# Kernel optimization log

Measured on AMD Instinct MI355X. Metric: run time of the kernel, lower is better.

The kernel has to match this reference:

```python
import jax, jax.numpy as jnp
import numpy as np

B, T, N, E = 4, 16, 1024, 16384
F_IN, H, FF, NH, L, C = 128, 256, 1024, 8, 2, 10
HD = H // NH
EPS = 1e-5


def setup_inputs() -> dict:
    key = jax.random.key(0)
    ks = jax.random.split(key, 12)
    g = lambda k, s: jax.random.normal(k, s, dtype=jnp.float32) * 0.02
    return {
        "x": jax.random.normal(ks[0], (B, T, N, F_IN), dtype=jnp.float32),
        "edge_index": jax.random.randint(ks[1], (B, T, 2, E), 0, N, dtype=jnp.int32),
        # GraphSAGE layer 1 (PyG SAGEConv: lin_l on mean-aggregated neighbors, lin_r on self)
        "sage1_Wl": g(ks[2], (F_IN, H)), "sage1_bl": jnp.zeros((H,), jnp.float32),
        "sage1_Wr": g(ks[3], (F_IN, H)),
        # GraphSAGE layer 2
        "sage2_Wl": g(ks[4], (H, H)), "sage2_bl": jnp.zeros((H,), jnp.float32),
        "sage2_Wr": g(ks[5], (H, H)),
        # TransformerEncoder, stacked over L layers
        "Wqkv": g(ks[6], (L, H, 3 * H)), "bqkv": jnp.zeros((L, 3 * H), jnp.float32),
        "Wo": g(ks[7], (L, H, H)), "bo": jnp.zeros((L, H), jnp.float32),
        "ln1_s": jnp.ones((L, H), jnp.float32), "ln1_b": jnp.zeros((L, H), jnp.float32),
        "W1": g(ks[8], (L, H, FF)), "b1": jnp.zeros((L, FF), jnp.float32),
        "W2": g(ks[9], (L, FF, H)), "b2": jnp.zeros((L, H), jnp.float32),
        "ln2_s": jnp.ones((L, H), jnp.float32), "ln2_b": jnp.zeros((L, H), jnp.float32),
        # final classifier
        "fc_W": g(ks[10], (H, C)), "fc_b": jnp.zeros((C,), jnp.float32),
    }


def _sage_conv(x, src, dst, Wl, bl, Wr):
    # mean neighbor aggregation: for each target node, mean of source features
    deg = jax.ops.segment_sum(jnp.ones((E,), x.dtype), dst, num_segments=N)
    agg = jax.ops.segment_sum(x[src], dst, num_segments=N)  # [N, F]
    agg = agg / jnp.clip(deg, 1.0)[:, None]
    return agg @ Wl + bl + x @ Wr


def _layernorm(x, s, b):
    m = jnp.mean(x, axis=-1, keepdims=True)
    v = jnp.var(x, axis=-1, keepdims=True)
    return (x - m) * jax.lax.rsqrt(v + EPS) * s + b


def _encoder_layer(h, Wqkv, bqkv, Wo, bo, ln1_s, ln1_b, W1, b1, W2, b2, ln2_s, ln2_b):
    # h: [B, T, H] -- post-norm (PyTorch default norm_first=False), relu FFN
    qkv = h @ Wqkv + bqkv  # [B, T, 3H]
    q, k, v = jnp.split(qkv, 3, axis=-1)
    sp = lambda t: t.reshape(B, T, NH, HD).transpose(0, 2, 1, 3)  # [B, NH, T, HD]
    q, k, v = sp(q), sp(k), sp(v)
    scores = jnp.einsum("bhqd,bhkd->bhqk", q, k) / np.sqrt(HD).astype(np.float32)
    attn = jax.nn.softmax(scores, axis=-1)
    ctx = jnp.einsum("bhqk,bhkd->bhqd", attn, v)
    ctx = ctx.transpose(0, 2, 1, 3).reshape(B, T, H)
    h = _layernorm(h + ctx @ Wo + bo, ln1_s, ln1_b)
    ffn = jax.nn.relu(h @ W1 + b1) @ W2 + b2
    return _layernorm(h + ffn, ln2_s, ln2_b)


def reference(x, edge_index, sage1_Wl, sage1_bl, sage1_Wr, sage2_Wl, sage2_bl,
              sage2_Wr, Wqkv, bqkv, Wo, bo, ln1_s, ln1_b, W1, b1, W2, b2,
              ln2_s, ln2_b, fc_W, fc_b):
    xf = x.reshape(B * T, N, F_IN)
    ef = edge_index.reshape(B * T, 2, E)

    def per_graph(xg, eg):
        src, dst = eg[0], eg[1]
        h = jax.nn.relu(_sage_conv(xg, src, dst, sage1_Wl, sage1_bl, sage1_Wr))
        h = _sage_conv(h, src, dst, sage2_Wl, sage2_bl, sage2_Wr)
        return jnp.mean(h, axis=0)  # mean-pool over nodes -> [H]

    emb = jax.vmap(per_graph)(xf, ef).reshape(B, T, H)

    h = emb
    for l in range(L):
        h = _encoder_layer(h, Wqkv[l], bqkv[l], Wo[l], bo[l], ln1_s[l], ln1_b[l],
                           W1[l], b1[l], W2[l], b2[l], ln2_s[l], ln2_b[l])
    return h[:, -1, :] @ fc_W + fc_b  # [B, C]
```

## Files before the change

### kernel.cpp

```cpp
#include <hip/hip_runtime.h>
#include <hip/hip_bf16.h>

#define Bc 4
#define Tc 16
#define Nc 1024
#define Ec 16384
#define FIN 128
#define Hc 256
#define FFc 1024
#define NHc 8
#define Lc 2
#define HDc 32
#define Gc 64
#define EPSc 1e-5f

typedef __bf16 v8bf __attribute__((ext_vector_type(8)));
typedef float v4f __attribute__((ext_vector_type(4)));

__global__ void pack_w_kernel(const float* __restrict__ Wl, const float* __restrict__ Wr,
                              __bf16* __restrict__ pH, __bf16* __restrict__ pL) {
    int bid = blockIdx.x;
    int t = threadIdx.x;
    int lane = t >> 3, j = t & 7;
    int kc = bid >> 4, nt = bid & 15;
    int k = kc * 32 + ((lane >> 4) << 3) + j;
    int n = nt * 16 + (lane & 15);
    float w = (k < 128) ? Wl[(size_t)k * Hc + n] : Wr[(size_t)(k - 128) * Hc + n];
    __bf16 hi = (__bf16)w;
    __bf16 lo = (__bf16)(w - (float)hi);
    pH[bid * 512 + t] = hi;
    pL[bid * 512 + t] = lo;
}

__global__ __launch_bounds__(1024) void csr_kernel(
        const int* __restrict__ ei, float* __restrict__ invdeg, float* __restrict__ cw,
        int* __restrict__ off, unsigned short* __restrict__ elist, float* __restrict__ uv) {
    __shared__ int degs[Nc];
    __shared__ float inv[Nc];
    __shared__ float cl[Nc];
    __shared__ int scan[Nc];
    int g = blockIdx.x, t = threadIdx.x;
    const int* src = ei + (size_t)g * 2 * Ec;
    const int* dst = src + Ec;
    if (t < 512) uv[g * 512 + t] = 0.f;
    degs[t] = 0; cl[t] = 0.f;
    __syncthreads();
    for (int e = t; e < Ec; e += 1024) atomicAdd(&degs[dst[e] & (Nc - 1)], 1);
    __syncthreads();
    float iv = 1.0f / fmaxf((float)degs[t], 1.0f);
    inv[t] = iv;
    invdeg[g * Nc + t] = iv;
    __syncthreads();
    for (int e = t; e < Ec; e += 1024) atomicAdd(&cl[src[e] & (Nc - 1)], inv[dst[e] & (Nc - 1)]);
    __syncthreads();
    cw[g * Nc + t] = cl[t];
    int own = degs[t];
    scan[t] = own;
    __syncthreads();
    for (int ofs = 1; ofs < 1024; ofs <<= 1) {
        int v = (t >= ofs) ? scan[t - ofs] : 0;
        __syncthreads();
        scan[t] += v;
        __syncthreads();
    }
    int excl = scan[t] - own;
    off[g * 1032 + t] = excl;
    if (t == 1023) off[g * 1032 + Nc] = scan[1023];
    degs[t] = excl;
    __syncthreads();
    for (int e = t; e < Ec; e += 1024) {
        int d = dst[e] & (Nc - 1);
        int slot = atomicAdd(&degs[d], 1);
        elist[(size_t)g * Ec + slot] = (unsigned short)(src[e] & (Nc - 1));
    }
}

__global__ __launch_bounds__(512) void sage_kernel(
        const float* __restrict__ x, const unsigned short* __restrict__ elist,
        const int* __restrict__ off, const float* __restrict__ invdeg,
        const float* __restrict__ cw, const __bf16* __restrict__ pH,
        const __bf16* __restrict__ pL, const float* __restrict__ bias,
        float* __restrict__ uv) {
    __shared__ float aggL[32 * 132];
    __shared__ float xL[32 * 132];
    __shared__ float lu[256], lv[256];
    int tid = threadIdx.x;
    int bid = blockIdx.x;
    int g = bid >> 5, cc = bid & 31, r0 = cc * 32;
    const unsigned short* el = elist + (size_t)g * Ec;
    const float* xg = x + (size_t)g * Nc * FIN;
    if (tid < 256) { lu[tid] = 0.f; lv[tid] = 0.f; }

    {
        int lr = tid >> 4, ch = tid & 15;
        int n = r0 + lr;
        int o0 = off[g * 1032 + n], o1 = off[g * 1032 + n + 1];
        float4 a0 = make_float4(0.f, 0.f, 0.f, 0.f);
        float4 a1 = make_float4(0.f, 0.f, 0.f, 0.f);
        const float* xc = xg + ch * 8;
        int e = o0;
        for (; e + 8 <= o1; e += 8) {
            int s[8];
#pragma unroll
            for (int j = 0; j < 8; ++j) s[j] = el[e + j];
            float4 v0[8], v1[8];
#pragma unroll
            for (int j = 0; j < 8; ++j) {
                const float4* xp = (const float4*)(xc + (size_t)s[j] * FIN);
                v0[j] = xp[0]; v1[j] = xp[1];
            }
#pragma unroll
            for (int j = 0; j < 8; ++j) {
                a0.x += v0[j].x; a0.y += v0[j].y; a0.z += v0[j].z; a0.w += v0[j].w;
                a1.x += v1[j].x; a1.y += v1[j].y; a1.z += v1[j].z; a1.w += v1[j].w;
            }
        }
        for (; e < o1; ++e) {
            const float4* xp = (const float4*)(xc + (size_t)el[e] * FIN);
            float4 v0 = xp[0], v1 = xp[1];
            a0.x += v0.x; a0.y += v0.y; a0.z += v0.z; a0.w += v0.w;
            a1.x += v1.x; a1.y += v1.y; a1.z += v1.z; a1.w += v1.w;
        }
        float iv = invdeg[g * Nc + n];
        float* dp = &aggL[lr * 132 + ch * 8];
        dp[0] = a0.x * iv; dp[1] = a0.y * iv; dp[2] = a0.z * iv; dp[3] = a0.w * iv;
        dp[4] = a1.x * iv; dp[5] = a1.y * iv; dp[6] = a1.z * iv; dp[7] = a1.w * iv;
    }
    for (int i = tid; i < 1024; i += 512) {
        int lr = i >> 5, kq = i & 31;
        *(float4*)&xL[lr * 132 + kq * 4] = *(const float4*)&xg[(size_t)(r0 + lr) * FIN + kq * 4];
    }
    __syncthreads();

    int w = tid >> 6, lane = tid & 63, quad = lane >> 4;
    int mt = w & 1, nh = w >> 1;
    int lrow = mt * 16 + (lane & 15);
    v4f acc[4];
#pragma unroll
    for (int i = 0; i < 4; ++i) acc[i] = (v4f)0.f;
    for (int kc = 0; kc < 8; ++kc) {
        const float* ap = (kc < 4) ? &aggL[lrow * 132 + kc * 32 + quad * 8]
                                   : &xL[lrow * 132 + (kc - 4) * 32 + quad * 8];
        float4 f0 = *(const float4*)ap;
        float4 f1 = *(const float4*)(ap + 4);
        float av[8] = {f0.x, f0.y, f0.z, f0.w, f1.x, f1.y, f1.z, f1.w};
        v8bf aH, aL;
#pragma unroll
        for (int j = 0; j < 8; ++j) {
            __bf16 hb = (__bf16)av[j];
            aH[j] = hb;
            aL[j] = (__bf16)(av[j] - (float)hb);
        }
#pragma unroll
        for (int i = 0; i < 4; ++i) {
            int nt = nh * 4 + i;
            v8bf bH = *(const v8bf*)(pH + ((size_t)(kc * 16 + nt) * 64 + lane) * 8);
            v8bf bL = *(const v8bf*)(pL + ((size_t)(kc * 16 + nt) * 64 + lane) * 8);
            acc[i] = __builtin_amdgcn_mfma_f32_16x16x32_bf16(aH, bH, acc[i], 0, 0, 0);
            acc[i] = __builtin_amdgcn_mfma_f32_16x16x32_bf16(aL, bH, acc[i], 0, 0, 0);
            acc[i] = __builtin_amdgcn_mfma_f32_16x16x32_bf16(aH, bL, acc[i], 0, 0, 0);
        }
    }

    float c4[4];
    int nb = g * Nc + r0 + mt * 16 + quad * 4;
#pragma unroll
    for (int r = 0; r < 4; ++r) c4[r] = cw[nb + r];
#pragma unroll
    for (int i = 0; i < 4; ++i) {
        int col = (nh * 4 + i) * 16 + (lane & 15);
        float bcol = bias[col];
        float su = 0.f, sv = 0.f;
#pragma unroll
        for (int r = 0; r < 4; ++r) {
            float val = fmaxf(acc[i][r] + bcol, 0.f);
            sv += val;
            su += c4[r] * val;
        }
        su += __shfl_xor(su, 16); sv += __shfl_xor(sv, 16);
        su += __shfl_xor(su, 32); sv += __shfl_xor(sv, 32);
        if (quad == 0) { atomicAdd(&lu[col], su); atomicAdd(&lv[col], sv); }
    }
    __syncthreads();
    if (tid < 256) {
        atomicAdd(&uv[g * 512 + tid], lu[tid]);
        atomicAdd(&uv[g * 512 + 256 + tid], lv[tid]);
    }
}

__global__ __launch_bounds__(512) void emb_kernel(
        const float* __restrict__ uv, const float* __restrict__ Wl2,
        const float* __restrict__ bl2, const float* __restrict__ Wr2,
        float* __restrict__ h) {
    __shared__ float s[512];
    __shared__ float r2[512];
    int g = blockIdx.x, tid = threadIdx.x;
    s[tid] = uv[g * 512 + tid] * (1.0f / Nc);
    __syncthreads();
    int col = tid & 255, p = tid >> 8;
    float val = 0.f;
    if (p == 0) { for (int k = 0; k < 256; ++k) val += s[k] * Wl2[(size_t)k * Hc + col]; }
    else        { for (int k = 0; k < 256; ++k) val += s[256 + k] * Wr2[(size_t)k * Hc + col]; }
    r2[tid] = val;
    __syncthreads();
    if (tid < 256) h[g * Hc + tid] = bl2[tid] + r2[tid] + r2[tid + 256];
}

__global__ __launch_bounds__(512) void qkv_kernel(
        const float* __restrict__ h, const float* __restrict__ Wqkv,
        const float* __restrict__ bqkv, float* __restrict__ qkv, int l) {
    __shared__ float hr[256];
    __shared__ float r2[512];
    int bid = blockIdx.x;
    int gi = bid / 3, seg = bid % 3;
    int tid = threadIdx.x;
    if (tid < 256) hr[tid] = h[gi * Hc + tid];
    __syncthreads();
    int col = seg * 256 + (tid & 255);
    int half = tid >> 8;
    const float* W = Wqkv + (size_t)l * Hc * 768;
    float val = 0.f;
    int k0 = half * 128;
    for (int k = 0; k < 128; ++k) val += hr[k0 + k] * W[(size_t)(k0 + k) * 768 + col];
    r2[tid] = val;
    __syncthreads();
    if (tid < 256) qkv[gi * 768 + col] = bqkv[(size_t)l * 768 + col] + r2[tid] + r2[tid + 256];
}

#define KVS 516
__global__ __launch_bounds__(256) void apl_kernel(
        const float* __restrict__ h, const float* __restrict__ qkvg,
        const float* __restrict__ Wo, const float* __restrict__ bo,
        const float* __restrict__ s1, const float* __restrict__ b1ln,
        float* __restrict__ h1buf, int l) {
    __shared__ float kv[16 * KVS];
    __shared__ float q[256];
    __shared__ float sc[8][17];
    __shared__ float ctx[256];
    __shared__ float red[256];
    int t = blockIdx.x, tid = threadIdx.x;
    int b = t >> 4;
    const float* qb = qkvg + (size_t)(b * 16) * 768;
    for (int i = tid; i < 8192; i += 256) {
        int j = i >> 9, d = i & 511;
        kv[j * KVS + d] = qb[(size_t)j * 768 + 256 + d];
    }
    q[tid] = qkvg[(size_t)t * 768 + tid];
    __syncthreads();
    if (tid < 128) {
        int hd = tid >> 4, j = tid & 15;
        float s = 0.f;
#pragma unroll
        for (int d = 0; d < 32; ++d) s += q[hd * 32 + d] * kv[j * KVS + hd * 32 + d];
        sc[hd][j] = s * 0.17677669529663687f;
    }
    __syncthreads();
    if (tid < 8) {
        float m = sc[tid][0];
        for (int j = 1; j < 16; ++j) m = fmaxf(m, sc[tid][j]);
        float e[16], sum = 0.f;
        for (int j = 0; j < 16; ++j) { e[j] = expf(sc[tid][j] - m); sum += e[j]; }
        float inv = 1.0f / sum;
        for (int j = 0; j < 16; ++j) sc[tid][j] = e[j] * inv;
    }
    __syncthreads();
    {
        int hd = tid >> 5, d = tid & 31;
        float o = 0.f;
#pragma unroll
        for (int j = 0; j < 16; ++j) o += sc[hd][j] * kv[j * KVS + 256 + hd * 32 + d];
        ctx[tid] = o;
    }
    __syncthreads();
    const float* W = Wo + (size_t)l * 65536;
    float val = h[(size_t)t * 256 + tid] + bo[(size_t)l * 256 + tid];
    for (int k = 0; k < 256; ++k) val += ctx[k] * W[(size_t)k * 256 + tid];
    red[tid] = val; __syncthreads();
    for (int s = 128; s > 0; s >>= 1) { if (tid < s) red[tid] += red[tid + s]; __syncthreads(); }
    float m1 = red[0] * (1.0f / 256.0f);
    __syncthreads();
    float d1 = val - m1;
    red[tid] = d1 * d1; __syncthreads();
    for (int s = 128; s > 0; s >>= 1) { if (tid < s) red[tid] += red[tid + s]; __syncthreads(); }
    float v1 = red[0] * (1.0f / 256.0f);
    h1buf[(size_t)t * 256 + tid] =
        d1 * rsqrtf(v1 + EPSc) * s1[(size_t)l * 256 + tid] + b1ln[(size_t)l * 256 + tid];
}

__global__ __launch_bounds__(256) void ffn1_kernel(
        const float* __restrict__ h1buf, const float* __restrict__ W1,
        const float* __restrict__ bf1, float* __restrict__ fL, int l) {
    __shared__ float hr[256];
    int bid = blockIdx.x;
    int t = bid >> 2, cg = bid & 3;
    int tid = threadIdx.x;
    hr[tid] = h1buf[(size_t)t * 256 + tid];
    __syncthreads();
    int col = cg * 256 + tid;
    const float* W = W1 + (size_t)l * 262144;
    float val = bf1[(size_t)l * 1024 + col];
    for (int k = 0; k < 256; ++k) val += hr[k] * W[(size_t)k * 1024 + col];
    fL[(size_t)t * 1024 + col] = fmaxf(val, 0.f);
}

__global__ __launch_bounds__(1024) void ffn2_ln_kernel(
        float* __restrict__ h, const float* __restrict__ h1buf, const float* __restrict__ fL,
        const float* __restrict__ W2, const float* __restrict__ bf2,
        const float* __restrict__ s2, const float* __restrict__ b2ln,
        const float* __restrict__ fcW, const float* __restrict__ fcb,
        float* __restrict__ out, int l, int last) {
    __shared__ float fs[1024];
    __shared__ float r4[1024];
    __shared__ float red[256];
    int t = blockIdx.x, tid = threadIdx.x;
    fs[tid] = fL[(size_t)t * 1024 + tid];
    __syncthreads();
    int col = tid & 255, kq = tid >> 8;
    const float* W = W2 + (size_t)l * 262144;
    float p = 0.f;
    int k0 = kq * 256;
    for (int k = 0; k < 256; ++k) p += fs[k0 + k] * W[(size_t)(k0 + k) * 256 + col];
    r4[tid] = p;
    __syncthreads();
    float val = 0.f;
    if (tid < 256) {
        val = h1buf[(size_t)t * 256 + tid] + bf2[(size_t)l * 256 + tid]
            + r4[tid] + r4[tid + 256] + r4[tid + 512] + r4[tid + 768];
        red[tid] = val;
    }
    __syncthreads();
    for (int s = 128; s > 0; s >>= 1) { if (tid < s) red[tid] += red[tid + s]; __syncthreads(); }
    float m2 = red[0] * (1.0f / 256.0f);
    __syncthreads();
    float d2 = (tid < 256) ? (val - m2) : 0.f;
    if (tid < 256) red[tid] = d2 * d2;
    __syncthreads();
    for (int s = 128; s > 0; s >>= 1) { if (tid < s) red[tid] += red[tid + s]; __syncthreads(); }
    float var2 = red[0] * (1.0f / 256.0f);
    float hn = 0.f;
    if (tid < 256) {
        hn = d2 * rsqrtf(var2 + EPSc) * s2[(size_t)l * 256 + tid] + b2ln[(size_t)l * 256 + tid];
        h[(size_t)t * 256 + tid] = hn;
    }
    if (last && (t & 15) == 15) {
        __syncthreads();
        if (tid < 256) red[tid] = hn;
        __syncthreads();
        if (tid < 10) {
            int b = t >> 4;
            float fv = fcb[tid];
            for (int k = 0; k < 256; ++k) fv += red[k] * fcW[(size_t)k * 10 + tid];
            out[b * 10 + tid] = fv;
        }
    }
}

extern "C" void kernel_launch(void* const* d_in, const int* in_sizes, int n_in,
                              void* d_out, int out_size, void* d_ws, size_t ws_size,
                              hipStream_t stream) {
    (void)in_sizes; (void)n_in; (void)out_size; (void)ws_size;
    const float* x    = (const float*)d_in[0];
    const int*   ei   = (const int*)d_in[1];
    const float* s1Wl = (const float*)d_in[2];
    const float* s1bl = (const float*)d_in[3];
    const float* s1Wr = (const float*)d_in[4];
    const float* s2Wl = (const float*)d_in[5];
    const float* s2bl = (const float*)d_in[6];
    const float* s2Wr = (const float*)d_in[7];
    const float* Wqkv = (const float*)d_in[8];
    const float* bqkv = (const float*)d_in[9];
    const float* Wo   = (const float*)d_in[10];
    const float* bo   = (const float*)d_in[11];
    const float* ln1s = (const float*)d_in[12];
    const float* ln1b = (const float*)d_in[13];
    const float* W1   = (const float*)d_in[14];
    const float* b1   = (const float*)d_in[15];
    const float* W2   = (const float*)d_in[16];
    const float* b2   = (const float*)d_in[17];
    const float* ln2s = (const float*)d_in[18];
    const float* ln2b = (const float*)d_in[19];
    const float* fcW  = (const float*)d_in[20];
    const float* fcb  = (const float*)d_in[21];

    char* ws = (char*)d_ws;
    __bf16*         packWH = (__bf16*)(ws + 0);
    __bf16*         packWL = (__bf16*)(ws + 131072);
    float*          invdeg = (float*)(ws + 262144);
    float*          cw     = (float*)(ws + 524288);
    int*            off    = (int*)(ws + 786432);
    unsigned short* elist  = (unsigned short*)(ws + 1050624);
    float*          uv     = (float*)(ws + 3147776);
    float*          h      = (float*)(ws + 3278848);
    float*          qkvg   = (float*)(ws + 3344384);
    float*          h1buf  = (float*)(ws + 3540992);
    float*          fLbuf  = (float*)(ws + 3606528);

    pack_w_kernel<<<128, 512, 0, stream>>>(s1Wl, s1Wr, packWH, packWL);
    csr_kernel<<<Gc, 1024, 0, stream>>>(ei, invdeg, cw, off, elist, uv);
    sage_kernel<<<Gc * 32, 512, 0, stream>>>(x, elist, off, invdeg, cw, packWH, packWL, s1bl, uv);
    emb_kernel<<<Gc, 512, 0, stream>>>(uv, s2Wl, s2bl, s2Wr, h);
    for (int l = 0; l < Lc; ++l) {
        qkv_kernel<<<Gc * 3, 512, 0, stream>>>(h, Wqkv, bqkv, qkvg, l);
        apl_kernel<<<Gc, 256, 0, stream>>>(h, qkvg, Wo, bo, ln1s, ln1b, h1buf, l);
        ffn1_kernel<<<Gc * 4, 256, 0, stream>>>(h1buf, W1, b1, fLbuf, l);
        ffn2_ln_kernel<<<Gc, 1024, 0, stream>>>(h, h1buf, fLbuf, W2, b2, ln2s, ln2b,
                                                fcW, fcb, (float*)d_out, l, l == Lc - 1);
    }
}
```

Before: 335.7 us.

## Use wavefront shuffle scan, interleave sage blocks, split-K apl and ffn1 matvecs

The CSR prefix scan replaces the log-step shared-memory scan, which had many block barriers, with a per-wavefront shuffle scan followed by a small cross-wave scan. The sage kernel's block-to-graph mapping is interleaved so consecutive blocks land on different graphs, which may spread the work more evenly. The apl and ffn1 kernels move to 512 threads and split the K dimension in half, with a shared-memory reduction, to double parallelism on these serial matvec loops. The cost is extra barriers and idle threads during the reduction phases.

Measured after the change: 313.3 us. 6.7% less time.

```diff
diff --git a/kernel.cpp b/kernel.cpp
--- a/kernel.cpp
+++ b/kernel.cpp
@@ -38,7 +38,7 @@
     __shared__ int degs[Nc];
     __shared__ float inv[Nc];
     __shared__ float cl[Nc];
-    __shared__ int scan[Nc];
+    __shared__ int wsum[16];
     int g = blockIdx.x, t = threadIdx.x;
     const int* src = ei + (size_t)g * 2 * Ec;
     const int* dst = src + Ec;
@@ -55,17 +55,29 @@
     __syncthreads();
     cw[g * Nc + t] = cl[t];
     int own = degs[t];
-    scan[t] = own;
-    __syncthreads();
-    for (int ofs = 1; ofs < 1024; ofs <<= 1) {
-        int v = (t >= ofs) ? scan[t - ofs] : 0;
-        __syncthreads();
-        scan[t] += v;
-        __syncthreads();
-    }
-    int excl = scan[t] - own;
+    int lane = t & 63, wv = t >> 6;
+    int val = own;
+#pragma unroll
+    for (int ofs = 1; ofs < 64; ofs <<= 1) {
+        int v = __shfl_up(val, ofs, 64);
+        if (lane >= ofs) val += v;
+    }
+    if (lane == 63) wsum[wv] = val;
+    __syncthreads();
+    if (wv == 0 && lane < 16) {
+        int wval = wsum[lane];
+#pragma unroll
+        for (int ofs = 1; ofs < 16; ofs <<= 1) {
+            int v = __shfl_up(wval, ofs, 64);
+            if (lane >= ofs) wval += v;
+        }
+        wsum[lane] = wval;
+    }
+    __syncthreads();
+    int incl = val + ((wv > 0) ? wsum[wv - 1] : 0);
+    int excl = incl - own;
     off[g * 1032 + t] = excl;
-    if (t == 1023) off[g * 1032 + Nc] = scan[1023];
+    if (t == 1023) off[g * 1032 + Nc] = incl;
     degs[t] = excl;
     __syncthreads();
     for (int e = t; e < Ec; e += 1024) {
@@ -86,7 +98,7 @@
     __shared__ float lu[256], lv[256];
     int tid = threadIdx.x;
     int bid = blockIdx.x;
-    int g = bid >> 5, cc = bid & 31, r0 = cc * 32;
+    int g = bid & 63, cc = bid >> 6, r0 = cc * 32;
     const unsigned short* el = elist + (size_t)g * Ec;
     const float* xg = x + (size_t)g * Nc * FIN;
     if (tid < 256) { lu[tid] = 0.f; lv[tid] = 0.f; }
@@ -228,7 +240,7 @@
 }
 
 #define KVS 516
-__global__ __launch_bounds__(256) void apl_kernel(
+__global__ __launch_bounds__(512) void apl_kernel(
         const float* __restrict__ h, const float* __restrict__ qkvg,
         const float* __restrict__ Wo, const float* __restrict__ bo,
         const float* __restrict__ s1, const float* __restrict__ b1ln,
@@ -237,15 +249,16 @@
     __shared__ float q[256];
     __shared__ float sc[8][17];
     __shared__ float ctx[256];
+    __shared__ float r2[512];
     __shared__ float red[256];
     int t = blockIdx.x, tid = threadIdx.x;
     int b = t >> 4;
     const float* qb = qkvg + (size_t)(b * 16) * 768;
-    for (int i = tid; i < 8192; i += 256) {
+    for (int i = tid; i < 8192; i += 512) {
         int j = i >> 9, d = i & 511;
         kv[j * KVS + d] = qb[(size_t)j * 768 + 256 + d];
     }
-    q[tid] = qkvg[(size_t)t * 768 + tid];
+    if (tid < 256) q[tid] = qkvg[(size_t)t * 768 + tid];
     __syncthreads();
     if (tid < 128) {
         int hd = tid >> 4, j = tid & 15;
@@ -264,7 +277,7 @@
         for (int j = 0; j < 16; ++j) sc[tid][j] = e[j] * inv;
     }
     __syncthreads();
-    {
+    if (tid < 256) {
         int hd = tid >> 5, d = tid & 31;
         float o = 0.f;
 #pragma unroll
@@ -272,35 +285,52 @@
         ctx[tid] = o;
     }
     __syncthreads();
+    int col = tid & 255, half = tid >> 8;
     const float* W = Wo + (size_t)l * 65536;
-    float val = h[(size_t)t * 256 + tid] + bo[(size_t)l * 256 + tid];
-    for (int k = 0; k < 256; ++k) val += ctx[k] * W[(size_t)k * 256 + tid];
-    red[tid] = val; __syncthreads();
+    float pv = 0.f;
+    int k0 = half * 128;
+    for (int k = 0; k < 128; ++k) pv += ctx[k0 + k] * W[(size_t)(k0 + k) * 256 + col];
+    r2[tid] = pv;
+    __syncthreads();
+    float val = 0.f;
+    if (tid < 256) {
+        val = h[(size_t)t * 256 + tid] + bo[(size_t)l * 256 + tid] + r2[tid] + r2[tid + 256];
+        red[tid] = val;
+    }
+    __syncthreads();
     for (int s = 128; s > 0; s >>= 1) { if (tid < s) red[tid] += red[tid + s]; __syncthreads(); }
     float m1 = red[0] * (1.0f / 256.0f);
     __syncthreads();
     float d1 = val - m1;
-    red[tid] = d1 * d1; __syncthreads();
+    if (tid < 256) red[tid] = d1 * d1;
+    __syncthreads();
     for (int s = 128; s > 0; s >>= 1) { if (tid < s) red[tid] += red[tid + s]; __syncthreads(); }
     float v1 = red[0] * (1.0f / 256.0f);
-    h1buf[(size_t)t * 256 + tid] =
-        d1 * rsqrtf(v1 + EPSc) * s1[(size_t)l * 256 + tid] + b1ln[(size_t)l * 256 + tid];
-}
-
-__global__ __launch_bounds__(256) void ffn1_kernel(
+    if (tid < 256)
+        h1buf[(size_t)t * 256 + tid] =
+            d1 * rsqrtf(v1 + EPSc) * s1[(size_t)l * 256 + tid] + b1ln[(size_t)l * 256 + tid];
+}
+
+__global__ __launch_bounds__(512) void ffn1_kernel(
         const float* __restrict__ h1buf, const float* __restrict__ W1,
         const float* __restrict__ bf1, float* __restrict__ fL, int l) {
     __shared__ float hr[256];
+    __shared__ float r2[512];
     int bid = blockIdx.x;
     int t = bid >> 2, cg = bid & 3;
     int tid = threadIdx.x;
-    hr[tid] = h1buf[(size_t)t * 256 + tid];
-    __syncthreads();
-    int col = cg * 256 + tid;
+    if (tid < 256) hr[tid] = h1buf[(size_t)t * 256 + tid];
+    __syncthreads();
+    int col = cg * 256 + (tid & 255);
+    int half = tid >> 8;
     const float* W = W1 + (size_t)l * 262144;
-    float val = bf1[(size_t)l * 1024 + col];
-    for (int k = 0; k < 256; ++k) val += hr[k] * W[(size_t)k * 1024 + col];
-    fL[(size_t)t * 1024 + col] = fmaxf(val, 0.f);
+    float val = 0.f;
+    int k0 = half * 128;
+    for (int k = 0; k < 128; ++k) val += hr[k0 + k] * W[(size_t)(k0 + k) * 1024 + col];
+    r2[tid] = val;
+    __syncthreads();
+    if (tid < 256)
+        fL[(size_t)t * 1024 + col] = fmaxf(bf1[(size_t)l * 1024 + col] + r2[tid] + r2[tid + 256], 0.f);
 }
 
 __global__ __launch_bounds__(1024) void ffn2_ln_kernel(
@@ -401,8 +431,8 @@
     emb_kernel<<<Gc, 512, 0, stream>>>(uv, s2Wl, s2bl, s2Wr, h);
     for (int l = 0; l < Lc; ++l) {
         qkv_kernel<<<Gc * 3, 512, 0, stream>>>(h, Wqkv, bqkv, qkvg, l);
-        apl_kernel<<<Gc, 256, 0, stream>>>(h, qkvg, Wo, bo, ln1s, ln1b, h1buf, l);
-        ffn1_kernel<<<Gc * 4, 256, 0, stream>>>(h1buf, W1, b1, fLbuf, l);
+        apl_kernel<<<Gc, 512, 0, stream>>>(h, qkvg, Wo, bo, ln1s, ln1b, h1buf, l);
+        ffn1_kernel<<<Gc * 4, 512, 0, stream>>>(h1buf, W1, b1, fLbuf, l);
         ffn2_ln_kernel<<<Gc, 1024, 0, stream>>>(h, h1buf, fLbuf, W2, b2, ln2s, ln2b,
                                                 fcW, fcb, (float*)d_out, l, l == Lc - 1);
     }
```

## Fuse prep kernels, retile SAGE GEMM, and merge transformer into one mega kernel

Applied to the files above, without the earlier changes.

Merges weight packing into the CSR build kernel and replaces the block-wide shared-memory scan with a wave-shuffle scan. The SAGE kernel now handles 64 rows per block, stores pre-split bf16 hi/lo operands in LDS, and drops the shared-memory reduction in favor of direct global atomics. The emb/qkv/attention/FFN/LayerNorm kernels across both layers are fused into one per-batch mega kernel using split-bf16 MFMA GEMMs, removing many launches. The trade-off is that the transformer now runs on only 4 blocks, which limits parallelism, and global atomic contention increases.

Result: slower. 355.7 us (+6.0%).

```diff
diff --git a/kernel.cpp b/kernel.cpp
--- a/kernel.cpp
+++ b/kernel.cpp
@@ -17,28 +17,29 @@
 typedef __bf16 v8bf __attribute__((ext_vector_type(8)));
 typedef float v4f __attribute__((ext_vector_type(4)));
 
-__global__ void pack_w_kernel(const float* __restrict__ Wl, const float* __restrict__ Wr,
-                              __bf16* __restrict__ pH, __bf16* __restrict__ pL) {
-    int bid = blockIdx.x;
-    int t = threadIdx.x;
-    int lane = t >> 3, j = t & 7;
-    int kc = bid >> 4, nt = bid & 15;
-    int k = kc * 32 + ((lane >> 4) << 3) + j;
-    int n = nt * 16 + (lane & 15);
-    float w = (k < 128) ? Wl[(size_t)k * Hc + n] : Wr[(size_t)(k - 128) * Hc + n];
-    __bf16 hi = (__bf16)w;
-    __bf16 lo = (__bf16)(w - (float)hi);
-    pH[bid * 512 + t] = hi;
-    pL[bid * 512 + t] = lo;
-}
-
-__global__ __launch_bounds__(1024) void csr_kernel(
-        const int* __restrict__ ei, float* __restrict__ invdeg, float* __restrict__ cw,
-        int* __restrict__ off, unsigned short* __restrict__ elist, float* __restrict__ uv) {
+__global__ __launch_bounds__(1024) void prep_kernel(
+        const int* __restrict__ ei, const float* __restrict__ Wl, const float* __restrict__ Wr,
+        float* __restrict__ invdeg, float* __restrict__ cw, int* __restrict__ off,
+        unsigned short* __restrict__ elist, float* __restrict__ uv,
+        __bf16* __restrict__ pH, __bf16* __restrict__ pL) {
     __shared__ int degs[Nc];
     __shared__ float inv[Nc];
     __shared__ float cl[Nc];
-    __shared__ int scan[Nc];
+    __shared__ int wsum[16];
+    if (blockIdx.x >= 64) {
+        int id = (blockIdx.x - 64) * 1024 + threadIdx.x;
+        int t = id & 511;
+        int bidOld = id >> 9;
+        int lane = t >> 3, j = t & 7;
+        int kc = bidOld >> 4, nt = bidOld & 15;
+        int k = kc * 32 + ((lane >> 4) << 3) + j;
+        int n = nt * 16 + (lane & 15);
+        float wv = (k < 128) ? Wl[(size_t)k * Hc + n] : Wr[(size_t)(k - 128) * Hc + n];
+        __bf16 hi = (__bf16)wv;
+        pH[id] = hi;
+        pL[id] = (__bf16)(wv - (float)hi);
+        return;
+    }
     int g = blockIdx.x, t = threadIdx.x;
     const int* src = ei + (size_t)g * 2 * Ec;
     const int* dst = src + Ec;
@@ -55,17 +56,29 @@
     __syncthreads();
     cw[g * Nc + t] = cl[t];
     int own = degs[t];
-    scan[t] = own;
-    __syncthreads();
-    for (int ofs = 1; ofs < 1024; ofs <<= 1) {
-        int v = (t >= ofs) ? scan[t - ofs] : 0;
-        __syncthreads();
-        scan[t] += v;
-        __syncthreads();
-    }
-    int excl = scan[t] - own;
+    int lane = t & 63, wv2 = t >> 6;
+    int val = own;
+#pragma unroll
+    for (int ofs = 1; ofs < 64; ofs <<= 1) {
+        int v = __shfl_up(val, ofs, 64);
+        if (lane >= ofs) val += v;
+    }
+    if (lane == 63) wsum[wv2] = val;
+    __syncthreads();
+    if (wv2 == 0 && lane < 16) {
+        int wval = wsum[lane];
+#pragma unroll
+        for (int ofs = 1; ofs < 16; ofs <<= 1) {
+            int v = __shfl_up(wval, ofs, 64);
+            if (lane >= ofs) wval += v;
+        }
+        wsum[lane] = wval;
+    }
+    __syncthreads();
+    int incl = val + ((wv2 > 0) ? wsum[wv2 - 1] : 0);
+    int excl = incl - own;
     off[g * 1032 + t] = excl;
-    if (t == 1023) off[g * 1032 + Nc] = scan[1023];
+    if (t == 1023) off[g * 1032 + Nc] = incl;
     degs[t] = excl;
     __syncthreads();
     for (int e = t; e < Ec; e += 1024) {
@@ -75,283 +88,279 @@
     }
 }
 
-__global__ __launch_bounds__(512) void sage_kernel(
+__global__ __launch_bounds__(512, 4) void sage_kernel(
         const float* __restrict__ x, const unsigned short* __restrict__ elist,
         const int* __restrict__ off, const float* __restrict__ invdeg,
         const float* __restrict__ cw, const __bf16* __restrict__ pH,
         const __bf16* __restrict__ pL, const float* __restrict__ bias,
         float* __restrict__ uv) {
-    __shared__ float aggL[32 * 132];
-    __shared__ float xL[32 * 132];
-    __shared__ float lu[256], lv[256];
-    int tid = threadIdx.x;
-    int bid = blockIdx.x;
-    int g = bid >> 5, cc = bid & 31, r0 = cc * 32;
+    __shared__ __bf16 AH[64 * 264];
+    __shared__ __bf16 AL[64 * 264];
+    int tid = threadIdx.x, bid = blockIdx.x;
+    int g = bid & 63, cc = bid >> 6, r0 = cc * 64;
     const unsigned short* el = elist + (size_t)g * Ec;
     const float* xg = x + (size_t)g * Nc * FIN;
-    if (tid < 256) { lu[tid] = 0.f; lv[tid] = 0.f; }
 
     {
-        int lr = tid >> 4, ch = tid & 15;
+        int lr = tid >> 3, ch = tid & 7;
         int n = r0 + lr;
         int o0 = off[g * 1032 + n], o1 = off[g * 1032 + n + 1];
-        float4 a0 = make_float4(0.f, 0.f, 0.f, 0.f);
-        float4 a1 = make_float4(0.f, 0.f, 0.f, 0.f);
-        const float* xc = xg + ch * 8;
+        float4 a0 = {0.f,0.f,0.f,0.f}, a1 = a0, a2 = a0, a3 = a0;
+        const float* xc = xg + ch * 16;
         int e = o0;
-        for (; e + 8 <= o1; e += 8) {
-            int s[8];
-#pragma unroll
-            for (int j = 0; j < 8; ++j) s[j] = el[e + j];
-            float4 v0[8], v1[8];
-#pragma unroll
-            for (int j = 0; j < 8; ++j) {
-                const float4* xp = (const float4*)(xc + (size_t)s[j] * FIN);
-                v0[j] = xp[0]; v1[j] = xp[1];
-            }
-#pragma unroll
-            for (int j = 0; j < 8; ++j) {
-                a0.x += v0[j].x; a0.y += v0[j].y; a0.z += v0[j].z; a0.w += v0[j].w;
-                a1.x += v1[j].x; a1.y += v1[j].y; a1.z += v1[j].z; a1.w += v1[j].w;
-            }
+        for (; e + 4 <= o1; e += 4) {
+            int s0 = el[e], s1 = el[e+1], s2 = el[e+2], s3 = el[e+3];
+            const float4* p0 = (const float4*)(xc + (size_t)s0 * FIN);
+            const float4* p1 = (const float4*)(xc + (size_t)s1 * FIN);
+            const float4* p2 = (const float4*)(xc + (size_t)s2 * FIN);
+            const float4* p3 = (const float4*)(xc + (size_t)s3 * FIN);
+            float4 v00=p0[0], v01=p0[1], v02=p0[2], v03=p0[3];
+            float4 v10=p1[0], v11=p1[1], v12=p1[2], v13=p1[3];
+            float4 v20=p2[0], v21=p2[1], v22=p2[2], v23=p2[3];
+            float4 v30=p3[0], v31=p3[1], v32=p3[2], v33=p3[3];
+            a0.x += v00.x+v10.x+v20.x+v30.x; a0.y += v00.y+v10.y+v20.y+v30.y;
+            a0.z += v00.z+v10.z+v20.z+v30.z; a0.w += v00.w+v10.w+v20.w+v30.w;
+            a1.x += v01.x+v11.x+v21.x+v31.x; a1.y += v01.y+v11.y+v21.y+v31.y;
+            a1.z += v01.z+v11.z+v21.z+v31.z; a1.w += v01.w+v11.w+v21.w+v31.w;
+            a2.x += v02.x+v12.x+v22.x+v32.x; a2.y += v02.y+v12.y+v22.y+v32.y;
+            a2.z += v02.z+v12.z+v22.z+v32.z; a2.w += v02.w+v12.w+v22.w+v32.w;
+            a3.x += v03.x+v13.x+v23.x+v33.x; a3.y += v03.y+v13.y+v23.y+v33.y;
+            a3.z += v03.z+v13.z+v23.z+v33.z; a3.w += v03.w+v13.w+v23.w+v33.w;
         }
         for (; e < o1; ++e) {
-            const float4* xp = (const float4*)(xc + (size_t)el[e] * FIN);
-            float4 v0 = xp[0], v1 = xp[1];
-            a0.x += v0.x; a0.y += v0.y; a0.z += v0.z; a0.w += v0.w;
-            a1.x += v1.x; a1.y += v1.y; a1.z += v1.z; a1.w += v1.w;
+            const float4* p = (const float4*)(xc + (size_t)el[e] * FIN);
+            float4 v0=p[0], v1=p[1], v2=p[2], v3=p[3];
+            a0.x+=v0.x; a0.y+=v0.y; a0.z+=v0.z; a0.w+=v0.w;
+            a1.x+=v1.x; a1.y+=v1.y; a1.z+=v1.z; a1.w+=v1.w;
+            a2.x+=v2.x; a2.y+=v2.y; a2.z+=v2.z; a2.w+=v2.w;
+            a3.x+=v3.x; a3.y+=v3.y; a3.z+=v3.z; a3.w+=v3.w;
         }
         float iv = invdeg[g * Nc + n];
-        float* dp = &aggL[lr * 132 + ch * 8];
-        dp[0] = a0.x * iv; dp[1] = a0.y * iv; dp[2] = a0.z * iv; dp[3] = a0.w * iv;
-        dp[4] = a1.x * iv; dp[5] = a1.y * iv; dp[6] = a1.z * iv; dp[7] = a1.w * iv;
-    }
-    for (int i = tid; i < 1024; i += 512) {
-        int lr = i >> 5, kq = i & 31;
-        *(float4*)&xL[lr * 132 + kq * 4] = *(const float4*)&xg[(size_t)(r0 + lr) * FIN + kq * 4];
-    }
-    __syncthreads();
-
-    int w = tid >> 6, lane = tid & 63, quad = lane >> 4;
-    int mt = w & 1, nh = w >> 1;
-    int lrow = mt * 16 + (lane & 15);
-    v4f acc[4];
-#pragma unroll
-    for (int i = 0; i < 4; ++i) acc[i] = (v4f)0.f;
+        float vals[16] = {a0.x*iv,a0.y*iv,a0.z*iv,a0.w*iv, a1.x*iv,a1.y*iv,a1.z*iv,a1.w*iv,
+                          a2.x*iv,a2.y*iv,a2.z*iv,a2.w*iv, a3.x*iv,a3.y*iv,a3.z*iv,a3.w*iv};
+        v8bf h0, h1v, l0, l1v;
+#pragma unroll
+        for (int i = 0; i < 8; ++i) {
+            __bf16 hb = (__bf16)vals[i];
+            h0[i] = hb; l0[i] = (__bf16)(vals[i] - (float)hb);
+            __bf16 hb2 = (__bf16)vals[i+8];
+            h1v[i] = hb2; l1v[i] = (__bf16)(vals[i+8] - (float)hb2);
+        }
+        __bf16* dh = &AH[lr * 264 + ch * 16];
+        __bf16* dl = &AL[lr * 264 + ch * 16];
+        *(v8bf*)dh = h0; *(v8bf*)(dh + 8) = h1v;
+        *(v8bf*)dl = l0; *(v8bf*)(dl + 8) = l1v;
+        const float4* xr = (const float4*)(xg + (size_t)n * FIN + ch * 16);
+        float4 x0 = xr[0], x1 = xr[1], x2 = xr[2], x3 = xr[3];
+        float xv[16] = {x0.x,x0.y,x0.z,x0.w, x1.x,x1.y,x1.z,x1.w,
+                        x2.x,x2.y,x2.z,x2.w, x3.x,x3.y,x3.z,x3.w};
+#pragma unroll
+        for (int i = 0; i < 8; ++i) {
+            __bf16 hb = (__bf16)xv[i];
+            h0[i] = hb; l0[i] = (__bf16)(xv[i] - (float)hb);
+            __bf16 hb2 = (__bf16)xv[i+8];
+            h1v[i] = hb2; l1v[i] = (__bf16)(xv[i+8] - (float)hb2);
+        }
+        dh = &AH[lr * 264 + 128 + ch * 16];
+        dl = &AL[lr * 264 + 128 + ch * 16];
+        *(v8bf*)dh = h0; *(v8bf*)(dh + 8) = h1v;
+        *(v8bf*)dl = l0; *(v8bf*)(dl + 8) = l1v;
+    }
+    __syncthreads();
+
+    int w = tid >> 6, lane = tid & 63, quad = lane >> 4, lm = lane & 15;
+    v4f acc[4][2];
+#pragma unroll
+    for (int m = 0; m < 4; ++m) { acc[m][0] = (v4f)0.f; acc[m][1] = (v4f)0.f; }
+    const v8bf* wpH = (const v8bf*)pH;
+    const v8bf* wpL = (const v8bf*)pL;
     for (int kc = 0; kc < 8; ++kc) {
-        const float* ap = (kc < 4) ? &aggL[lrow * 132 + kc * 32 + quad * 8]
-                                   : &xL[lrow * 132 + (kc - 4) * 32 + quad * 8];
-        float4 f0 = *(const float4*)ap;
-        float4 f1 = *(const float4*)(ap + 4);
-        float av[8] = {f0.x, f0.y, f0.z, f0.w, f1.x, f1.y, f1.z, f1.w};
-        v8bf aH, aL;
-#pragma unroll
-        for (int j = 0; j < 8; ++j) {
-            __bf16 hb = (__bf16)av[j];
-            aH[j] = hb;
-            aL[j] = (__bf16)(av[j] - (float)hb);
-        }
-#pragma unroll
-        for (int i = 0; i < 4; ++i) {
-            int nt = nh * 4 + i;
-            v8bf bH = *(const v8bf*)(pH + ((size_t)(kc * 16 + nt) * 64 + lane) * 8);
-            v8bf bL = *(const v8bf*)(pL + ((size_t)(kc * 16 + nt) * 64 + lane) * 8);
-            acc[i] = __builtin_amdgcn_mfma_f32_16x16x32_bf16(aH, bH, acc[i], 0, 0, 0);
-            acc[i] = __builtin_amdgcn_mfma_f32_16x16x32_bf16(aL, bH, acc[i], 0, 0, 0);
-            acc[i] = __builtin_amdgcn_mfma_f32_16x16x32_bf16(aH, bL, acc[i], 0, 0, 0);
-        }
-    }
-
-    float c4[4];
-    int nb = g * Nc + r0 + mt * 16 + quad * 4;
-#pragma unroll
-    for (int r = 0; r < 4; ++r) c4[r] = cw[nb + r];
-#pragma unroll
-    for (int i = 0; i < 4; ++i) {
-        int col = (nh * 4 + i) * 16 + (lane & 15);
+        v8bf bH0 = wpH[(kc * 16 + 2 * w    ) * 64 + lane];
+        v8bf bL0 = wpL[(kc * 16 + 2 * w    ) * 64 + lane];
+        v8bf bH1 = wpH[(kc * 16 + 2 * w + 1) * 64 + lane];
+        v8bf bL1 = wpL[(kc * 16 + 2 * w + 1) * 64 + lane];
+#pragma unroll
+        for (int mt = 0; mt < 4; ++mt) {
+            int ao = (mt * 16 + lm) * 264 + kc * 32 + quad * 8;
+            v8bf aH = *(const v8bf*)&AH[ao];
+            v8bf aL = *(const v8bf*)&AL[ao];
+            acc[mt][0] = __builtin_amdgcn_mfma_f32_16x16x32_bf16(aH, bH0, acc[mt][0], 0, 0, 0);
+            acc[mt][0] = __builtin_amdgcn_mfma_f32_16x16x32_bf16(aL, bH0, acc[mt][0], 0, 0, 0);
+            acc[mt][0] = __builtin_amdgcn_mfma_f32_16x16x32_bf16(aH, bL0, acc[mt][0], 0, 0, 0);
+            acc[mt][1] = __builtin_amdgcn_mfma_f32_16x16x32_bf16(aH, bH1, acc[mt][1], 0, 0, 0);
+            acc[mt][1] = __builtin_amdgcn_mfma_f32_16x16x32_bf16(aL, bH1, acc[mt][1], 0, 0, 0);
+            acc[mt][1] = __builtin_amdgcn_mfma_f32_16x16x32_bf16(aH, bL1, acc[mt][1], 0, 0, 0);
+        }
+    }
+#pragma unroll
+    for (int j = 0; j < 2; ++j) {
+        int col = (2 * w + j) * 16 + lm;
         float bcol = bias[col];
         float su = 0.f, sv = 0.f;
 #pragma unroll
-        for (int r = 0; r < 4; ++r) {
-            float val = fmaxf(acc[i][r] + bcol, 0.f);
-            sv += val;
-            su += c4[r] * val;
+        for (int mt = 0; mt < 4; ++mt) {
+            int nb = g * Nc + r0 + mt * 16 + quad * 4;
+#pragma unroll
+            for (int r = 0; r < 4; ++r) {
+                float val = fmaxf(acc[mt][j][r] + bcol, 0.f);
+                sv += val;
+                su += cw[nb + r] * val;
+            }
         }
         su += __shfl_xor(su, 16); sv += __shfl_xor(sv, 16);
         su += __shfl_xor(su, 32); sv += __shfl_xor(sv, 32);
-        if (quad == 0) { atomicAdd(&lu[col], su); atomicAdd(&lv[col], sv); }
-    }
-    __syncthreads();
-    if (tid < 256) {
-        atomicAdd(&uv[g * 512 + tid], lu[tid]);
-        atomicAdd(&uv[g * 512 + 256 + tid], lv[tid]);
-    }
-}
-
-__global__ __launch_bounds__(512) void emb_kernel(
-        const float* __restrict__ uv, const float* __restrict__ Wl2,
-        const float* __restrict__ bl2, const float* __restrict__ Wr2,
-        float* __restrict__ h) {
-    __shared__ float s[512];
-    __shared__ float r2[512];
-    int g = blockIdx.x, tid = threadIdx.x;
-    s[tid] = uv[g * 512 + tid] * (1.0f / Nc);
-    __syncthreads();
-    int col = tid & 255, p = tid >> 8;
-    float val = 0.f;
-    if (p == 0) { for (int k = 0; k < 256; ++k) val += s[k] * Wl2[(size_t)k * Hc + col]; }
-    else        { for (int k = 0; k < 256; ++k) val += s[256 + k] * Wr2[(size_t)k * Hc + col]; }
-    r2[tid] = val;
-    __syncthreads();
-    if (tid < 256) h[g * Hc + tid] = bl2[tid] + r2[tid] + r2[tid + 256];
-}
-
-__global__ __launch_bounds__(512) void qkv_kernel(
-        const float* __restrict__ h, const float* __restrict__ Wqkv,
-        const float* __restrict__ bqkv, float* __restrict__ qkv, int l) {
-    __shared__ float hr[256];
-    __shared__ float r2[512];
-    int bid = blockIdx.x;
-    int gi = bid / 3, seg = bid % 3;
-    int tid = threadIdx.x;
-    if (tid < 256) hr[tid] = h[gi * Hc + tid];
-    __syncthreads();
-    int col = seg * 256 + (tid & 255);
-    int half = tid >> 8;
-    const float* W = Wqkv + (size_t)l * Hc * 768;
-    float val = 0.f;
-    int k0 = half * 128;
-    for (int k = 0; k < 128; ++k) val += hr[k0 + k] * W[(size_t)(k0 + k) * 768 + col];
-    r2[tid] = val;
-    __syncthreads();
-    if (tid < 256) qkv[gi * 768 + col] = bqkv[(size_t)l * 768 + col] + r2[tid] + r2[tid + 256];
-}
-
-#define KVS 516
-__global__ __launch_bounds__(256) void apl_kernel(
-        const float* __restrict__ h, const float* __restrict__ qkvg,
+        if (quad == 0) {
+            atomicAdd(&uv[g * 512 + col], su);
+            atomicAdd(&uv[g * 512 + 256 + col], sv);
+        }
+    }
+}
+
+__device__ __forceinline__ void gemm16(
+        const float* __restrict__ A, int As,
+        const float* __restrict__ W, int N, int K,
+        const float* __restrict__ bias,
+        float* __restrict__ O, int Os, int relu, int accum, int tid) {
+    int w = tid >> 6, lane = tid & 63, quad = lane >> 4, lm = lane & 15;
+    int ntot = N >> 4, kcs = K >> 5;
+    for (int nt = w; nt < ntot; nt += 16) {
+        v4f acc = (v4f)0.f;
+        for (int kc = 0; kc < kcs; ++kc) {
+            const float* ap = A + lm * As + kc * 32 + quad * 8;
+            float4 f0 = *(const float4*)ap;
+            float4 f1 = *(const float4*)(ap + 4);
+            float av[8] = {f0.x, f0.y, f0.z, f0.w, f1.x, f1.y, f1.z, f1.w};
+            v8bf aH, aL, bH, bL;
+            const float* wp = W + (size_t)(kc * 32 + quad * 8) * N + nt * 16 + lm;
+#pragma unroll
+            for (int j = 0; j < 8; ++j) {
+                __bf16 ah = (__bf16)av[j];
+                aH[j] = ah; aL[j] = (__bf16)(av[j] - (float)ah);
+                float wv = wp[(size_t)j * N];
+                __bf16 wh = (__bf16)wv;
+                bH[j] = wh; bL[j] = (__bf16)(wv - (float)wh);
+            }
+            acc = __builtin_amdgcn_mfma_f32_16x16x32_bf16(aH, bH, acc, 0, 0, 0);
+            acc = __builtin_amdgcn_mfma_f32_16x16x32_bf16(aL, bH, acc, 0, 0, 0);
+            acc = __builtin_amdgcn_mfma_f32_16x16x32_bf16(aH, bL, acc, 0, 0, 0);
+        }
+        int col = nt * 16 + lm;
+        float bv = bias ? bias[col] : 0.f;
+#pragma unroll
+        for (int r = 0; r < 4; ++r) {
+            int tok = quad * 4 + r;
+            float val = acc[r] + bv;
+            if (relu) val = fmaxf(val, 0.f);
+            if (accum) O[tok * Os + col] += val;
+            else       O[tok * Os + col] = val;
+        }
+    }
+}
+
+__device__ __forceinline__ void ln16(const float* __restrict__ pre, const float* __restrict__ res,
+                                     const float* __restrict__ sc_, const float* __restrict__ bi,
+                                     float* __restrict__ out, int tid) {
+    int w = tid >> 6, lane = tid & 63;
+    float4 pv = *(const float4*)&pre[w * 260 + lane * 4];
+    float4 rv = *(const float4*)&res[w * 260 + lane * 4];
+    float x0 = pv.x + rv.x, x1 = pv.y + rv.y, x2 = pv.z + rv.z, x3 = pv.w + rv.w;
+    float s = x0 + x1 + x2 + x3;
+    float q = x0*x0 + x1*x1 + x2*x2 + x3*x3;
+#pragma unroll
+    for (int o = 1; o < 64; o <<= 1) { s += __shfl_xor(s, o); q += __shfl_xor(q, o); }
+    float m = s * (1.0f / 256.0f);
+    float var = q * (1.0f / 256.0f) - m * m;
+    float rstd = rsqrtf(var + EPSc);
+    float4 sv = *(const float4*)&sc_[lane * 4];
+    float4 bv = *(const float4*)&bi[lane * 4];
+    float4 ov;
+    ov.x = (x0 - m) * rstd * sv.x + bv.x;
+    ov.y = (x1 - m) * rstd * sv.y + bv.y;
+    ov.z = (x2 - m) * rstd * sv.z + bv.z;
+    ov.w = (x3 - m) * rstd * sv.w + bv.w;
+    *(float4*)&out[w * 260 + lane * 4] = ov;
+}
+
+__global__ __launch_bounds__(1024) void mega_kernel(
+        const float* __restrict__ uv,
+        const float* __restrict__ Wl2, const float* __restrict__ bl2, const float* __restrict__ Wr2,
+        const float* __restrict__ Wqkv, const float* __restrict__ bqkv,
         const float* __restrict__ Wo, const float* __restrict__ bo,
-        const float* __restrict__ s1, const float* __restrict__ b1ln,
-        float* __restrict__ h1buf, int l) {
-    __shared__ float kv[16 * KVS];
-    __shared__ float q[256];
-    __shared__ float sc[8][17];
-    __shared__ float ctx[256];
-    __shared__ float red[256];
-    int t = blockIdx.x, tid = threadIdx.x;
-    int b = t >> 4;
-    const float* qb = qkvg + (size_t)(b * 16) * 768;
-    for (int i = tid; i < 8192; i += 256) {
-        int j = i >> 9, d = i & 511;
-        kv[j * KVS + d] = qb[(size_t)j * 768 + 256 + d];
-    }
-    q[tid] = qkvg[(size_t)t * 768 + tid];
-    __syncthreads();
-    if (tid < 128) {
-        int hd = tid >> 4, j = tid & 15;
-        float s = 0.f;
-#pragma unroll
-        for (int d = 0; d < 32; ++d) s += q[hd * 32 + d] * kv[j * KVS + hd * 32 + d];
-        sc[hd][j] = s * 0.17677669529663687f;
-    }
-    __syncthreads();
-    if (tid < 8) {
-        float m = sc[tid][0];
-        for (int j = 1; j < 16; ++j) m = fmaxf(m, sc[tid][j]);
-        float e[16], sum = 0.f;
-        for (int j = 0; j < 16; ++j) { e[j] = expf(sc[tid][j] - m); sum += e[j]; }
-        float inv = 1.0f / sum;
-        for (int j = 0; j < 16; ++j) sc[tid][j] = e[j] * inv;
-    }
-    __syncthreads();
-    {
-        int hd = tid >> 5, d = tid & 31;
-        float o = 0.f;
-#pragma unroll
-        for (int j = 0; j < 16; ++j) o += sc[hd][j] * kv[j * KVS + 256 + hd * 32 + d];
-        ctx[tid] = o;
-    }
-    __syncthreads();
-    const float* W = Wo + (size_t)l * 65536;
-    float val = h[(size_t)t * 256 + tid] + bo[(size_t)l * 256 + tid];
-    for (int k = 0; k < 256; ++k) val += ctx[k] * W[(size_t)k * 256 + tid];
-    red[tid] = val; __syncthreads();
-    for (int s = 128; s > 0; s >>= 1) { if (tid < s) red[tid] += red[tid + s]; __syncthreads(); }
-    float m1 = red[0] * (1.0f / 256.0f);
-    __syncthreads();
-    float d1 = val - m1;
-    red[tid] = d1 * d1; __syncthreads();
-    for (int s = 128; s > 0; s >>= 1) { if (tid < s) red[tid] += red[tid + s]; __syncthreads(); }
-    float v1 = red[0] * (1.0f / 256.0f);
-    h1buf[(size_t)t * 256 + tid] =
-        d1 * rsqrtf(v1 + EPSc) * s1[(size_t)l * 256 + tid] + b1ln[(size_t)l * 256 + tid];
-}
-
-__global__ __launch_bounds__(256) void ffn1_kernel(
-        const float* __restrict__ h1buf, const float* __restrict__ W1,
-        const float* __restrict__ bf1, float* __restrict__ fL, int l) {
-    __shared__ float hr[256];
-    int bid = blockIdx.x;
-    int t = bid >> 2, cg = bid & 3;
-    int tid = threadIdx.x;
-    hr[tid] = h1buf[(size_t)t * 256 + tid];
-    __syncthreads();
-    int col = cg * 256 + tid;
-    const float* W = W1 + (size_t)l * 262144;
-    float val = bf1[(size_t)l * 1024 + col];
-    for (int k = 0; k < 256; ++k) val += hr[k] * W[(size_t)k * 1024 + col];
-    fL[(size_t)t * 1024 + col] = fmaxf(val, 0.f);
-}
-
-__global__ __launch_bounds__(1024) void ffn2_ln_kernel(
-        float* __restrict__ h, const float* __restrict__ h1buf, const float* __restrict__ fL,
-        const float* __restrict__ W2, const float* __restrict__ bf2,
-        const float* __restrict__ s2, const float* __restrict__ b2ln,
+        const float* __restrict__ ln1s, const float* __restrict__ ln1b,
+        const float* __restrict__ W1, const float* __restrict__ b1,
+        const float* __restrict__ W2, const float* __restrict__ b2,
+        const float* __restrict__ ln2s, const float* __restrict__ ln2b,
         const float* __restrict__ fcW, const float* __restrict__ fcb,
-        float* __restrict__ out, int l, int last) {
-    __shared__ float fs[1024];
-    __shared__ float r4[1024];
-    __shared__ float red[256];
-    int t = blockIdx.x, tid = threadIdx.x;
-    fs[tid] = fL[(size_t)t * 1024 + tid];
-    __syncthreads();
-    int col = tid & 255, kq = tid >> 8;
-    const float* W = W2 + (size_t)l * 262144;
-    float p = 0.f;
-    int k0 = kq * 256;
-    for (int k = 0; k < 256; ++k) p += fs[k0 + k] * W[(size_t)(k0 + k) * 256 + col];
-    r4[tid] = p;
-    __syncthreads();
-    float val = 0.f;
-    if (tid < 256) {
-        val = h1buf[(size_t)t * 256 + tid] + bf2[(size_t)l * 256 + tid]
-            + r4[tid] + r4[tid + 256] + r4[tid + 512] + r4[tid + 768];
-        red[tid] = val;
-    }
-    __syncthreads();
-    for (int s = 128; s > 0; s >>= 1) { if (tid < s) red[tid] += red[tid + s]; __syncthreads(); }
-    float m2 = red[0] * (1.0f / 256.0f);
-    __syncthreads();
-    float d2 = (tid < 256) ? (val - m2) : 0.f;
-    if (tid < 256) red[tid] = d2 * d2;
-    __syncthreads();
-    for (int s = 128; s > 0; s >>= 1) { if (tid < s) red[tid] += red[tid + s]; __syncthreads(); }
-    float var2 = red[0] * (1.0f / 256.0f);
-    float hn = 0.f;
-    if (tid < 256) {
-        hn = d2 * rsqrtf(var2 + EPSc) * s2[(size_t)l * 256 + tid] + b2ln[(size_t)l * 256 + tid];
-        h[(size_t)t * 256 + tid] = hn;
-    }
-    if (last && (t & 15) == 15) {
-        __syncthreads();
-        if (tid < 256) red[tid] = hn;
-        __syncthreads();
-        if (tid < 10) {
-            int b = t >> 4;
-            float fv = fcb[tid];
-            for (int k = 0; k < 256; ++k) fv += red[k] * fcW[(size_t)k * 10 + tid];
-            out[b * 10 + tid] = fv;
-        }
+        float* __restrict__ out) {
+    __shared__ float h[16 * 260];
+    __shared__ float big[16 * 1028];
+    __shared__ float ctx[16 * 260];
+    __shared__ float pre[16 * 260];
+    __shared__ float h1[16 * 260];
+    __shared__ float sc[2048];
+    int b = blockIdx.x, tid = threadIdx.x;
+
+    for (int i = tid; i < 16 * 512; i += 1024) {
+        int tok = i >> 9, k = i & 511;
+        big[tok * 516 + k] = uv[(size_t)(b * 16 + tok) * 512 + k] * (1.0f / 1024.0f);
+    }
+    __syncthreads();
+    gemm16(big,       516, Wl2, 256, 256, bl2,     h, 260, 0, 0, tid);
+    __syncthreads();
+    gemm16(big + 256, 516, Wr2, 256, 256, nullptr, h, 260, 0, 1, tid);
+    __syncthreads();
+
+    for (int l = 0; l < Lc; ++l) {
+        gemm16(h, 260, Wqkv + (size_t)l * Hc * 768, 768, 256, bqkv + l * 768, big, 772, 0, 0, tid);
+        __syncthreads();
+#pragma unroll
+        for (int rep = 0; rep < 2; ++rep) {
+            int idx = rep * 1024 + tid;
+            int hd = idx >> 8, qt = (idx >> 4) & 15, kt = idx & 15;
+            float s = 0.f;
+#pragma unroll
+            for (int d = 0; d < 32; ++d)
+                s += big[qt * 772 + hd * 32 + d] * big[kt * 772 + 256 + hd * 32 + d];
+            sc[idx] = s * 0.17677669529663687f;
+        }
+        __syncthreads();
+        if (tid < 128) {
+            int base = tid * 16;
+            float m = sc[base];
+            for (int j = 1; j < 16; ++j) m = fmaxf(m, sc[base + j]);
+            float ev[16], sum = 0.f;
+            for (int j = 0; j < 16; ++j) { ev[j] = expf(sc[base + j] - m); sum += ev[j]; }
+            float inv = 1.0f / sum;
+            for (int j = 0; j < 16; ++j) sc[base + j] = ev[j] * inv;
+        }
+        __syncthreads();
+#pragma unroll
+        for (int rep = 0; rep < 4; ++rep) {
+            int idx = rep * 1024 + tid;
+            int qt = idx >> 8, c = idx & 255;
+            int hd = c >> 5, d = c & 31;
+            float o = 0.f;
+#pragma unroll
+            for (int j = 0; j < 16; ++j)
+                o += sc[hd * 256 + qt * 16 + j] * big[j * 772 + 512 + hd * 32 + d];
+            ctx[qt * 260 + c] = o;
+        }
+        __syncthreads();
+        gemm16(ctx, 260, Wo + (size_t)l * 65536, 256, 256, bo + l * 256, pre, 260, 0, 0, tid);
+        __syncthreads();
+        ln16(pre, h, ln1s + l * 256, ln1b + l * 256, h1, tid);
+        __syncthreads();
+        gemm16(h1, 260, W1 + (size_t)l * 262144, 1024, 256, b1 + l * 1024, big, 1028, 1, 0, tid);
+        __syncthreads();
+        gemm16(big, 1028, W2 + (size_t)l * 262144, 256, 1024, b2 + l * 256, pre, 260, 0, 0, tid);
+        __syncthreads();
+        ln16(pre, h1, ln2s + l * 256, ln2b + l * 256, h, tid);
+        __syncthreads();
+    }
+    if (tid < 10) {
+        float v = fcb[tid];
+        for (int k = 0; k < 256; ++k) v += h[15 * 260 + k] * fcW[(size_t)k * 10 + tid];
+        out[b * 10 + tid] = v;
     }
 }
 
@@ -383,27 +392,17 @@
     const float* fcb  = (const float*)d_in[21];
 
     char* ws = (char*)d_ws;
-    __bf16*         packWH = (__bf16*)(ws + 0);
-    __bf16*         packWL = (__bf16*)(ws + 131072);
+    __bf16*         pH     = (__bf16*)(ws + 0);
+    __bf16*         pL     = (__bf16*)(ws + 131072);
     float*          invdeg = (float*)(ws + 262144);
     float*          cw     = (float*)(ws + 524288);
     int*            off    = (int*)(ws + 786432);
     unsigned short* elist  = (unsigned short*)(ws + 1050624);
     float*          uv     = (float*)(ws + 3147776);
-    float*          h      = (float*)(ws + 3278848);
-    float*          qkvg   = (float*)(ws + 3344384);
-    float*          h1buf  = (float*)(ws + 3540992);
-    float*          fLbuf  = (float*)(ws + 3606528);
-
-    pack_w_kernel<<<128, 512, 0, stream>>>(s1Wl, s1Wr, packWH, packWL);
-    csr_kernel<<<Gc, 1024, 0, stream>>>(ei, invdeg, cw, off, elist, uv);
-    sage_kernel<<<Gc * 32, 512, 0, stream>>>(x, elist, off, invdeg, cw, packWH, packWL, s1bl, uv);
-    emb_kernel<<<Gc, 512, 0, stream>>>(uv, s2Wl, s2bl, s2Wr, h);
-    for (int l = 0; l < Lc; ++l) {
-        qkv_kernel<<<Gc * 3, 512, 0, stream>>>(h, Wqkv, bqkv, qkvg, l);
-        apl_kernel<<<Gc, 256, 0, stream>>>(h, qkvg, Wo, bo, ln1s, ln1b, h1buf, l);
-        ffn1_kernel<<<Gc * 4, 256, 0, stream>>>(h1buf, W1, b1, fLbuf, l);
-        ffn2_ln_kernel<<<Gc, 1024, 0, stream>>>(h, h1buf, fLbuf, W2, b2, ln2s, ln2b,
-                                                fcW, fcb, (float*)d_out, l, l == Lc - 1);
-    }
-}
+
+    prep_kernel<<<128, 1024, 0, stream>>>(ei, s1Wl, s1Wr, invdeg, cw, off, elist, uv, pH, pL);
+    sage_kernel<<<Gc * 16, 512, 0, stream>>>(x, elist, off, invdeg, cw, pH, pL, s1bl, uv);
+    mega_kernel<<<Bc, 1024, 0, stream>>>(uv, s2Wl, s2bl, s2Wr, Wqkv, bqkv, Wo, bo,
+                                         ln1s, ln1b, W1, b1, W2, b2, ln2s, ln2b,
+                                         fcW, fcb, (float*)d_out);
+}
```
